# Performance work log

Measured on AMD Instinct MI355X. Metric: run time of the kernel, lower is better.

## Reference

```python
import jax, jax.numpy as jnp
import numpy as np

N, K, D = 8192, 64, 256          # nodes, edges per dst node, feat_dim
RATE = 0.5                        # denoise_topK_rate
SET0 = int(K * (1.0 - RATE))      # edges dropped per row (lowest keep-prob)


def setup_inputs() -> dict:
    key = jax.random.key(0)
    ks = jax.random.split(key, 6)
    # K unique, sorted neighbors per row (sorted => pair ordering matches
    # torch's row-major nonzero() on a dense adjacency)
    nbr = jax.vmap(lambda k: jax.random.permutation(k, N)[:K])(
        jax.random.split(ks[0], N))
    nbr = jnp.sort(nbr, axis=1).astype(jnp.int32)
    vals = jax.random.uniform(ks[1], (N, K), minval=0.1, maxval=1.0)
    adj = jnp.zeros((N, N), jnp.float32).at[jnp.arange(N)[:, None], nbr].set(vals)
    feat = jax.random.normal(ks[2], (N, D), dtype=jnp.float32)
    # keep_cls params: Linear(D, D//2) -> PReLU(D//2) -> Linear(D//2, 2)
    W1 = jax.random.normal(ks[3], (D, D // 2), dtype=jnp.float32) / np.float32(np.sqrt(D))
    b1 = jnp.zeros((D // 2,), jnp.float32)
    prelu_a = jnp.full((D // 2,), 0.25, jnp.float32)  # torch PReLU default init
    W2 = jax.random.normal(ks[4], (D // 2, 2), dtype=jnp.float32) / np.float32(np.sqrt(D // 2))
    b2 = jnp.zeros((2,), jnp.float32)
    return {"adj": adj, "feat": feat, "nbr_idx": nbr, "dst_num": N,
            "W1": W1, "b1": b1, "prelu_a": prelu_a, "W2": W2, "b2": b2}


def reference(adj, feat, nbr_idx, dst_num, W1, b1, prelu_a, W2, b2):
    dst = dst_num  # == adj.shape[0]; every dst row has exactly K nonzeros
    rows = jnp.arange(dst, dtype=jnp.int32)[:, None]            # [dst,1]
    pair_src = jnp.repeat(jnp.arange(dst, dtype=jnp.int32), K)  # [E]
    pair_dst = nbr_idx.reshape(-1)                              # [E]
    pair_list = jnp.stack([pair_src, pair_dst], axis=1)         # [E,2]
    before_edge_num = jnp.float32(pair_list.shape[0]) / dst

    # edge MLP on feature differences
    diff = feat[pair_src] - feat[pair_dst]                      # [E,D]
    h = diff @ W1 + b1
    h = jnp.where(h >= 0, h, prelu_a * h)                       # PReLU
    prob_arr = jax.nn.softmax(h @ W2 + b2, axis=1)              # [E,2]

    # segmented (per-dst-row) argsort of keep-prob; drop SET0 lowest
    p1 = prob_arr[:, 1].reshape(dst, K)                         # [dst,K]
    order = jnp.argsort(p1, axis=1)                             # ascending
    drop_cols = jnp.take_along_axis(nbr_idx, order[:, :SET0], axis=1)
    adj2 = adj.at[rows, drop_cols].set(0.0)
    left_row = (rows * K + order[:, SET0:]).reshape(-1)         # kept edge ids
    after_edge_num = jnp.count_nonzero(adj2).astype(jnp.float32) / dst

    # degree-normalize
    degrees = jnp.sum(adj2, axis=1)
    new_adj = adj2 / (degrees[:, None] + 1e-6)
    return (new_adj, feat, prob_arr, pair_list, before_edge_num,
            after_edge_num, left_row)
```

## Files before the change

kernel.cpp:

```cpp
#include <hip/hip_runtime.h>
#include <cmath>

#define NN 8192
#define KK 64
#define DD 256
#define HH 128
#define SET0V 32
#define EE (NN*KK)

typedef float f4_t __attribute__((ext_vector_type(4)));

static constexpr size_t OFF_ADJ  = 0;
static constexpr size_t OFF_FEAT = (size_t)NN * NN;
static constexpr size_t OFF_PROB = OFF_FEAT + (size_t)NN * DD;
static constexpr size_t OFF_PAIR = OFF_PROB + (size_t)EE * 2;
static constexpr size_t OFF_BEF  = OFF_PAIR + (size_t)EE * 2;
static constexpr size_t OFF_AFT  = OFF_BEF + 1;
static constexpr size_t OFF_LEFT = OFF_AFT + 1;

__global__ __launch_bounds__(128) void k_g(const float* __restrict__ feat,
                                           const float* __restrict__ W1,
                                           double* __restrict__ g,
                                           f4_t* __restrict__ out_feat,
                                           float* __restrict__ out_scal) {
  __shared__ float sf[8 * DD];
  int j = threadIdx.x;
  int n0 = blockIdx.x * 8;
  const f4_t* fsrc = (const f4_t*)(feat + (size_t)n0 * DD);
  f4_t* fdst = (f4_t*)sf;
  f4_t* odst = out_feat + (size_t)n0 * DD / 4;
#pragma unroll
  for (int t = 0; t < 4; t++) {
    f4_t v = fsrc[j + t * 128];
    fdst[j + t * 128] = v;
    __builtin_nontemporal_store(v, odst + j + t * 128);
  }
  if (blockIdx.x == 0 && j == 0) {
    out_scal[0] = 64.0f;
    out_scal[1] = 32.0f;
  }
  __syncthreads();
  double acc[8];
#pragma unroll
  for (int n = 0; n < 8; n++) acc[n] = 0.0;
  for (int k = 0; k < DD; k += 4) {
    double w0 = (double)W1[(k + 0) * HH + j];
    double w1 = (double)W1[(k + 1) * HH + j];
    double w2 = (double)W1[(k + 2) * HH + j];
    double w3 = (double)W1[(k + 3) * HH + j];
#pragma unroll
    for (int n = 0; n < 8; n++) {
      f4_t f = *(const f4_t*)&sf[n * DD + k];
      acc[n] += (double)f.x * w0;
      acc[n] += (double)f.y * w1;
      acc[n] += (double)f.z * w2;
      acc[n] += (double)f.w * w3;
    }
  }
#pragma unroll
  for (int n = 0; n < 8; n++) g[(size_t)(n0 + n) * HH + j] = acc[n];
}

__global__ __launch_bounds__(256) void k_main(
    const double* __restrict__ g, const int* __restrict__ nbr,
    const float* __restrict__ b1, const float* __restrict__ b2,
    const float* __restrict__ pa, const float* __restrict__ W2,
    const float* __restrict__ adj, float* __restrict__ out_adj,
    float* __restrict__ out_prob, float* __restrict__ out_pair,
    float* __restrict__ out_left) {
  int wave = threadIdx.x >> 6;
  int lane = threadIdx.x & 63;
  int r = blockIdx.x * 4 + wave;
  int q = lane >> 4;
  int s = lane & 15;

  const int* nrow = nbr + r * KK;
  int c_mine = nrow[lane];
  float v = __builtin_nontemporal_load(&adj[(size_t)r * NN + c_mine]);

  f4_t* row4 = (f4_t*)(out_adj + (size_t)r * NN);
  const f4_t z = {0.f, 0.f, 0.f, 0.f};

  double grb[8], aa[8], w0c[8], w1c[8];
  const double* gr = g + (size_t)r * HH + s * 8;
#pragma unroll
  for (int d = 0; d < 8; d++) {
    int dim = s * 8 + d;
    grb[d] = gr[d] + (double)b1[dim];
    aa[d]  = (double)pa[dim];
    w0c[d] = (double)W2[2 * dim];
    w1c[d] = (double)W2[2 * dim + 1];
  }

  double st0 = 0.0, st1 = 0.0;
  for (int grp = 0; grp < 16; grp++) {
    __builtin_nontemporal_store(z, row4 + lane + (2 * grp) * 64);
    __builtin_nontemporal_store(z, row4 + lane + (2 * grp + 1) * 64);

    int c = nrow[grp * 4 + q];
    const double* gc = g + (size_t)c * HH + s * 8;
    double t0 = 0.0, t1 = 0.0;
#pragma unroll
    for (int d = 0; d < 8; d++) {
      double h = grb[d] - gc[d];
      h = h >= 0.0 ? h : aa[d] * h;
      t0 += h * w0c[d];
      t1 += h * w1c[d];
    }
#pragma unroll
    for (int m = 1; m < 16; m <<= 1) {
      t0 += __shfl_xor(t0, m, 16);
      t1 += __shfl_xor(t1, m, 16);
    }
    if (s == grp) { st0 = t0; st1 = t1; }
  }
  int src = ((lane & 3) << 4) | (lane >> 2);
  double T0 = __shfl(st0, src, 64);
  double T1 = __shfl(st1, src, 64);
  double l0 = T0 + (double)b2[0];
  double l1 = T1 + (double)b2[1];
  double dkey = l1 - l0;

  size_t e = (size_t)r * KK + lane;
  float dm = (float)(l0 > l1 ? l0 : l1);
  float e0 = expf((float)l0 - dm), e1 = expf((float)l1 - dm);
  float inv = 1.0f / (e0 + e1);
  *(float2*)(out_prob + 2 * e) = make_float2(e0 * inv, e1 * inv);
  *(float2*)(out_pair + 2 * e) = make_float2((float)r, (float)c_mine);

  __shared__ double sp[4][64];
  __shared__ double sv[4][64];
  sp[wave][lane] = dkey;
  __syncthreads();
  int rank = 0;
#pragma unroll 8
  for (int j = 0; j < KK; j++) {
    double qq = sp[wave][j];
    rank += (int)((qq < dkey) || (qq == dkey && j < lane));
  }
  bool kept = rank >= SET0V;
  sv[wave][lane] = kept ? (double)v : 0.0;
  __syncthreads();
  double deg = 0.0;
#pragma unroll 8
  for (int j = 0; j < KK; j++) deg += sv[wave][j];
  if (kept) {
    out_adj[(size_t)r * NN + c_mine] = (float)((double)v / (deg + 1e-6));
    out_left[(size_t)r * SET0V + (rank - SET0V)] = (float)(r * KK + lane);
  }
}

extern "C" void kernel_launch(void* const* d_in, const int* in_sizes, int n_in,
                              void* d_out, int out_size, void* d_ws, size_t ws_size,
                              hipStream_t stream) {
  const float* adj  = (const float*)d_in[0];
  const float* feat = (const float*)d_in[1];
  const int*   nbr  = (const int*)d_in[2];
  const float* W1   = (const float*)d_in[4];
  const float* b1   = (const float*)d_in[5];
  const float* pa   = (const float*)d_in[6];
  const float* W2   = (const float*)d_in[7];
  const float* b2   = (const float*)d_in[8];
  float* out = (float*)d_out;

  double* g = (double*)d_ws;

  hipLaunchKernelGGL(k_g, dim3(1024), dim3(128), 0, stream,
                     feat, W1, g, (f4_t*)(out + OFF_FEAT), out + OFF_BEF);
  hipLaunchKernelGGL(k_main, dim3(2048), dim3(256), 0, stream,
                     g, nbr, b1, b2, pa, W2, adj,
                     out + OFF_ADJ, out + OFF_PROB, out + OFF_PAIR,
                     out + OFF_LEFT);
}
```

Baseline: 494.2 us.

## Compute edge MLP in fp32 with fp64 fallback when ranking margins are tight

Result: slower. 519.1 us (+5.1%).

```diff
diff --git a/kernel.cpp b/kernel.cpp
--- a/kernel.cpp
+++ b/kernel.cpp
@@ -18,9 +18,12 @@
 static constexpr size_t OFF_AFT  = OFF_BEF + 1;
 static constexpr size_t OFF_LEFT = OFF_AFT + 1;
 
+#define MARGIN 1e-4f
+
 __global__ __launch_bounds__(128) void k_g(const float* __restrict__ feat,
                                            const float* __restrict__ W1,
                                            double* __restrict__ g,
+                                           float* __restrict__ g32,
                                            f4_t* __restrict__ out_feat,
                                            float* __restrict__ out_scal) {
   __shared__ float sf[8 * DD];
@@ -58,11 +61,15 @@
     }
   }
 #pragma unroll
-  for (int n = 0; n < 8; n++) g[(size_t)(n0 + n) * HH + j] = acc[n];
+  for (int n = 0; n < 8; n++) {
+    g[(size_t)(n0 + n) * HH + j]   = acc[n];
+    g32[(size_t)(n0 + n) * HH + j] = (float)acc[n];
+  }
 }
 
 __global__ __launch_bounds__(256) void k_main(
-    const double* __restrict__ g, const int* __restrict__ nbr,
+    const double* __restrict__ g, const float* __restrict__ g32,
+    const int* __restrict__ nbr,
     const float* __restrict__ b1, const float* __restrict__ b2,
     const float* __restrict__ pa, const float* __restrict__ W2,
     const float* __restrict__ adj, float* __restrict__ out_adj,
@@ -81,29 +88,29 @@
   f4_t* row4 = (f4_t*)(out_adj + (size_t)r * NN);
   const f4_t z = {0.f, 0.f, 0.f, 0.f};
 
-  double grb[8], aa[8], w0c[8], w1c[8];
-  const double* gr = g + (size_t)r * HH + s * 8;
+  float grb[8], aa[8], w0c[8], w1c[8];
+  const float* gr32 = g32 + (size_t)r * HH + s * 8;
 #pragma unroll
   for (int d = 0; d < 8; d++) {
     int dim = s * 8 + d;
-    grb[d] = gr[d] + (double)b1[dim];
-    aa[d]  = (double)pa[dim];
-    w0c[d] = (double)W2[2 * dim];
-    w1c[d] = (double)W2[2 * dim + 1];
-  }
-
-  double st0 = 0.0, st1 = 0.0;
+    grb[d] = gr32[d] + b1[dim];
+    aa[d]  = pa[dim];
+    w0c[d] = W2[2 * dim];
+    w1c[d] = W2[2 * dim + 1];
+  }
+
+  float st0 = 0.f, st1 = 0.f;
   for (int grp = 0; grp < 16; grp++) {
     __builtin_nontemporal_store(z, row4 + lane + (2 * grp) * 64);
     __builtin_nontemporal_store(z, row4 + lane + (2 * grp + 1) * 64);
 
     int c = nrow[grp * 4 + q];
-    const double* gc = g + (size_t)c * HH + s * 8;
-    double t0 = 0.0, t1 = 0.0;
+    const float* gc = g32 + (size_t)c * HH + s * 8;
+    float t0 = 0.f, t1 = 0.f;
 #pragma unroll
     for (int d = 0; d < 8; d++) {
-      double h = grb[d] - gc[d];
-      h = h >= 0.0 ? h : aa[d] * h;
+      float h = grb[d] - gc[d];
+      h = h >= 0.f ? h : aa[d] * h;
       t0 += h * w0c[d];
       t1 += h * w1c[d];
     }
@@ -115,37 +122,80 @@
     if (s == grp) { st0 = t0; st1 = t1; }
   }
   int src = ((lane & 3) << 4) | (lane >> 2);
-  double T0 = __shfl(st0, src, 64);
-  double T1 = __shfl(st1, src, 64);
-  double l0 = T0 + (double)b2[0];
-  double l1 = T1 + (double)b2[1];
-  double dkey = l1 - l0;
+  float T0 = __shfl(st0, src, 64);
+  float T1 = __shfl(st1, src, 64);
+  float l0 = T0 + b2[0];
+  float l1 = T1 + b2[1];
+  float dkey = l1 - l0;
 
   size_t e = (size_t)r * KK + lane;
-  float dm = (float)(l0 > l1 ? l0 : l1);
-  float e0 = expf((float)l0 - dm), e1 = expf((float)l1 - dm);
+  float dm = l0 > l1 ? l0 : l1;
+  float e0 = expf(l0 - dm), e1 = expf(l1 - dm);
   float inv = 1.0f / (e0 + e1);
   *(float2*)(out_prob + 2 * e) = make_float2(e0 * inv, e1 * inv);
   *(float2*)(out_pair + 2 * e) = make_float2((float)r, (float)c_mine);
 
-  __shared__ double sp[4][64];
-  __shared__ double sv[4][64];
-  sp[wave][lane] = dkey;
-  __syncthreads();
   int rank = 0;
-#pragma unroll 8
-  for (int j = 0; j < KK; j++) {
-    double qq = sp[wave][j];
+  float mg = 1e30f;
+#pragma unroll 7
+  for (int off = 1; off < 64; off++) {
+    int j = (lane + off) & 63;
+    float qq = __shfl(dkey, j, 64);
     rank += (int)((qq < dkey) || (qq == dkey && j < lane));
-  }
+    mg = fminf(mg, fabsf(qq - dkey));
+  }
+#pragma unroll
+  for (int m = 1; m < 64; m <<= 1) mg = fminf(mg, __shfl_xor(mg, m, 64));
+
+  if (mg < MARGIN) {
+    double grb6[8], aa6[8], w06[8], w16[8];
+    const double* gr6 = g + (size_t)r * HH + s * 8;
+#pragma unroll
+    for (int d = 0; d < 8; d++) {
+      int dim = s * 8 + d;
+      grb6[d] = gr6[d] + (double)b1[dim];
+      aa6[d]  = (double)pa[dim];
+      w06[d]  = (double)W2[2 * dim];
+      w16[d]  = (double)W2[2 * dim + 1];
+    }
+    double s0 = 0.0, s1 = 0.0;
+    for (int grp = 0; grp < 16; grp++) {
+      int c = nrow[grp * 4 + q];
+      const double* gc = g + (size_t)c * HH + s * 8;
+      double t0 = 0.0, t1 = 0.0;
+#pragma unroll
+      for (int d = 0; d < 8; d++) {
+        double h = grb6[d] - gc[d];
+        h = h >= 0.0 ? h : aa6[d] * h;
+        t0 += h * w06[d];
+        t1 += h * w16[d];
+      }
+#pragma unroll
+      for (int m = 1; m < 16; m <<= 1) {
+        t0 += __shfl_xor(t0, m, 16);
+        t1 += __shfl_xor(t1, m, 16);
+      }
+      if (s == grp) { s0 = t0; s1 = t1; }
+    }
+    double D0 = __shfl(s0, src, 64);
+    double D1 = __shfl(s1, src, 64);
+    double dk64 = (D1 + (double)b2[1]) - (D0 + (double)b2[0]);
+    rank = 0;
+    for (int off = 1; off < 64; off++) {
+      int j = (lane + off) & 63;
+      double qq = __shfl(dk64, j, 64);
+      rank += (int)((qq < dk64) || (qq == dk64 && j < lane));
+    }
+  }
+
   bool kept = rank >= SET0V;
-  sv[wave][lane] = kept ? (double)v : 0.0;
-  __syncthreads();
-  double deg = 0.0;
-#pragma unroll 8
-  for (int j = 0; j < KK; j++) deg += sv[wave][j];
+  double dv = kept ? (double)v : 0.0;
+#pragma unroll
+  for (int m = 1; m < 64; m <<= 1) dv += __shfl_xor(dv, m, 64);
+
+  __builtin_amdgcn_s_waitcnt(0);
   if (kept) {
-    out_adj[(size_t)r * NN + c_mine] = (float)((double)v / (deg + 1e-6));
+    out_adj[(size_t)r * NN + c_mine] = (float)((double)v / (dv + 1e-6));
     out_left[(size_t)r * SET0V + (rank - SET0V)] = (float)(r * KK + lane);
   }
 }
@@ -163,12 +213,13 @@
   const float* b2   = (const float*)d_in[8];
   float* out = (float*)d_out;
 
-  double* g = (double*)d_ws;
+  double* g  = (double*)d_ws;
+  float* g32 = (float*)(g + (size_t)NN * HH);
 
   hipLaunchKernelGGL(k_g, dim3(1024), dim3(128), 0, stream,
-                     feat, W1, g, (f4_t*)(out + OFF_FEAT), out + OFF_BEF);
+                     feat, W1, g, g32, (f4_t*)(out + OFF_FEAT), out + OFF_BEF);
   hipLaunchKernelGGL(k_main, dim3(2048), dim3(256), 0, stream,
-                     g, nbr, b1, b2, pa, W2, adj,
+                     g, g32, nbr, b1, b2, pa, W2, adj,
                      out + OFF_ADJ, out + OFF_PROB, out + OFF_PAIR,
                      out + OFF_LEFT);
 }
```
